# Optimization experiments

Hardware: AMD Instinct MI355X
Metric: run time of the kernel (lower is better)

The kernel has to match this reference:

```python
import jax, jax.numpy as jnp
from jax import lax
import numpy as np

INIT_DIST = 1e10  # matches torch.ones(B,N) * 10000000000.0


def farthest_point_sample(xyz, npoint):
    """xyz: [B, N, 3] float. Returns idx [B, npoint] int32 (RAN=False seed = index 1)."""
    B, N, _ = xyz.shape
    dist0 = jnp.full((B, N), INIT_DIST, dtype=xyz.dtype)
    far0 = jnp.ones((B,), dtype=jnp.int32)  # RAN=False -> torch.randint(1, 2) == 1

    def step(carry, _):
        distance, farthest = carry
        # gather current centroid: [B, 1, 3]
        centroid = jnp.take_along_axis(xyz, farthest[:, None, None].astype(jnp.int32) * jnp.ones((1, 1, 3), jnp.int32), axis=1)
        d = jnp.sum((xyz - centroid) ** 2, axis=-1)        # [B, N]
        distance = jnp.minimum(distance, d)                 # masked update dist < distance
        new_far = jnp.argmax(distance, axis=-1).astype(jnp.int32)
        return (distance, new_far), farthest

    (_, _), idx = lax.scan(step, (dist0, far0), None, length=npoint)
    return idx.T  # [B, npoint]


def index_points(points, idx):
    """points: [B, N, C], idx: [B, S] -> [B, S, C]"""
    B = points.shape[0]
    return points[jnp.arange(B)[:, None], idx]


def setup_inputs() -> dict:
    key = jax.random.key(0)
    xyz = jax.random.normal(key, (32, 32768, 3), dtype=jnp.float32)
    return {"xyz": xyz, "npoint": 4096}


def reference(xyz, npoint):
    idx = farthest_point_sample(xyz, npoint)      # [B, npoint] int32
    sampled = index_points(xyz, idx)              # [B, npoint, 3]
    return idx, sampled
```

## Files before the change

kernel.cpp:

```cpp
#include <hip/hip_runtime.h>


#define BATCH  32
#define NPTS   32768
#define NPOINT 4096
#define NT     1024
#define NCH    16

__global__ __launch_bounds__(NT, 1)
__attribute__((amdgpu_num_vgpr(128)))
void fps_kernel(
    const float* __restrict__ xyz,
    float* __restrict__ out_idx,
    float* __restrict__ out_xyz)
{
#pragma clang fp contract(off)
    __shared__ float pz_lds[NPTS];
    __shared__ unsigned int s_val[3];
    __shared__ int s_idx[3];

    const int b   = blockIdx.x;
    const int tid = threadIdx.x;
    const float* base = xyz + (size_t)b * NPTS * 3;

    float px[NCH * 2], py[NCH * 2], dist[NCH * 2];
#pragma unroll
    for (int c = 0; c < NCH; ++c) {
#pragma unroll
        for (int j = 0; j < 2; ++j) {
            const int i = c * 2 + j;
            const int g = c * 2048 + 2 * tid + j;
            px[i] = base[g * 3 + 0];
            py[i] = base[g * 3 + 1];
            pz_lds[g] = base[g * 3 + 2];
            dist[i] = 1e10f;
        }
    }
    if (tid == 0) {
        s_val[0] = 0u; s_val[1] = 0u; s_val[2] = 0u;
        s_idx[0] = 0x7fffffff; s_idx[1] = 0x7fffffff; s_idx[2] = 0x7fffffff;
    }
    __syncthreads();

    int w = 1;
    int p = 0;

    for (int k = 0; k < NPOINT; ++k) {
        const float cx = base[w * 3 + 0];
        const float cy = base[w * 3 + 1];
        const float cz = base[w * 3 + 2];
        if (tid == 0) {
            out_idx[(size_t)b * NPOINT + k] = (float)w;
            float* o = out_xyz + ((size_t)b * NPOINT + k) * 3;
            o[0] = cx; o[1] = cy; o[2] = cz;
        }

        float best = -1.0f;
        int   lc   = 63;
#pragma unroll
        for (int c = 0; c < NCH; ++c) {
            const float2 zz = *(const float2*)&pz_lds[c * 2048 + 2 * tid];
            const float pzv[2] = { zz.x, zz.y };
#pragma unroll
            for (int j = 0; j < 2; ++j) {
                const int i = c * 2 + j;
                const float dx = px[i] - cx;
                const float dy = py[i] - cy;
                const float dz = pzv[j] - cz;
                const float d  = fmaf(dz, dz, fmaf(dx, dx, dy * dy));
                const float nd = fminf(dist[i], d);
                dist[i] = nd;
                if (nd > best) { best = nd; lc = 2 * c + j; }
            }
        }

        float m = best;
#pragma unroll
        for (int off = 1; off < 64; off <<= 1)
            m = fmaxf(m, __shfl_xor(m, off, 64));
        if ((tid & 63) == 0)
            atomicMax(&s_val[p], __float_as_uint(m));
        __syncthreads();
        const float M = __uint_as_float(s_val[p]);

        if (best == M) {
            const int bi = (lc >> 1) * 2048 + 2 * tid + (lc & 1);
            atomicMin(&s_idx[p], bi);
        }
        __syncthreads();
        w = s_idx[p];
        const int pn2 = (p >= 1) ? (p - 1) : 2;
        if (tid == 0) { s_val[pn2] = 0u; s_idx[pn2] = 0x7fffffff; }
        p = (p == 2) ? 0 : (p + 1);
    }
}

extern "C" void kernel_launch(void* const* d_in, const int* in_sizes, int n_in,
                              void* d_out, int out_size, void* d_ws, size_t ws_size,
                              hipStream_t stream) {
    const float* xyz = (const float*)d_in[0];
    float* out = (float*)d_out;
    float* out_idx = out;
    float* out_xyz = out + (size_t)BATCH * NPOINT;

    fps_kernel<<<BATCH, NT, 0, stream>>>(xyz, out_idx, out_xyz);
}
```

Baseline: 8.764 ms.

## Stream packed xy from workspace each iteration and use DPP wave max

A pre-pass packs x,y into a float2 workspace. The main kernel now reloads x,y from global memory (L2 or cache) with float4 loads on every iteration instead of holding them in registers. This frees VGPRs by dropping the 128-register cap, and the centroid z is read from LDS. The shuffle-based wave max reduction is replaced with DPP row operations, with the reduction result taken from lane 63. A fallback kernel keeps the old register-resident path for when the workspace is too small. The cost is extra global memory traffic inside each of the many serial iterations.

Result: faster. 8.144 ms (-7.1%).

```diff
diff --git a/kernel.cpp b/kernel.cpp
--- a/kernel.cpp
+++ b/kernel.cpp
@@ -6,11 +6,31 @@
 #define NPOINT 4096
 #define NT     1024
 #define NCH    16
-
-__global__ __launch_bounds__(NT, 1)
-__attribute__((amdgpu_num_vgpr(128)))
-void fps_kernel(
+#define WS_NEEDED ((size_t)BATCH * NPTS * 8)
+
+#define DPP1(x, ctrl, rm) __builtin_amdgcn_update_dpp((x), (x), (ctrl), (rm), 0xf, false)
+
+__device__ __forceinline__ float wave_max_dpp(float v) {
+    unsigned int u = __float_as_uint(v);
+    u = __float_as_uint(fmaxf(__uint_as_float(u), __uint_as_float(DPP1(u, 0xB1, 0xf))));
+    u = __float_as_uint(fmaxf(__uint_as_float(u), __uint_as_float(DPP1(u, 0x4E, 0xf))));
+    u = __float_as_uint(fmaxf(__uint_as_float(u), __uint_as_float(DPP1(u, 0x141, 0xf))));
+    u = __float_as_uint(fmaxf(__uint_as_float(u), __uint_as_float(DPP1(u, 0x140, 0xf))));
+    u = __float_as_uint(fmaxf(__uint_as_float(u), __uint_as_float(DPP1(u, 0x142, 0xa))));
+    u = __float_as_uint(fmaxf(__uint_as_float(u), __uint_as_float(DPP1(u, 0x143, 0xc))));
+    return __uint_as_float(u);
+}
+
+__global__ __launch_bounds__(256) void pack_xy(
+    const float* __restrict__ xyz, float2* __restrict__ ws)
+{
+    const int i = blockIdx.x * 256 + threadIdx.x;
+    ws[i] = make_float2(xyz[(size_t)i * 3 + 0], xyz[(size_t)i * 3 + 1]);
+}
+
+__global__ __launch_bounds__(NT, 1) void fps_kernel(
     const float* __restrict__ xyz,
+    const float2* __restrict__ wsxy,
     float* __restrict__ out_idx,
     float* __restrict__ out_xyz)
 {
@@ -22,18 +42,17 @@
     const int b   = blockIdx.x;
     const int tid = threadIdx.x;
     const float* base = xyz + (size_t)b * NPTS * 3;
-
-    float px[NCH * 2], py[NCH * 2], dist[NCH * 2];
+    const float2* xy  = wsxy + (size_t)b * NPTS;
+    const float4* xy4 = (const float4*)xy;
+
+    float dist[NCH * 2];
 #pragma unroll
     for (int c = 0; c < NCH; ++c) {
 #pragma unroll
         for (int j = 0; j < 2; ++j) {
-            const int i = c * 2 + j;
             const int g = c * 2048 + 2 * tid + j;
-            px[i] = base[g * 3 + 0];
-            py[i] = base[g * 3 + 1];
             pz_lds[g] = base[g * 3 + 2];
-            dist[i] = 1e10f;
+            dist[c * 2 + j] = 1e10f;
         }
     }
     if (tid == 0) {
@@ -46,9 +65,9 @@
     int p = 0;
 
     for (int k = 0; k < NPOINT; ++k) {
-        const float cx = base[w * 3 + 0];
-        const float cy = base[w * 3 + 1];
-        const float cz = base[w * 3 + 2];
+        const float2 cxy = xy[w];
+        const float cz = pz_lds[w];
+        const float cx = cxy.x, cy = cxy.y;
         if (tid == 0) {
             out_idx[(size_t)b * NPOINT + k] = (float)w;
             float* o = out_xyz + ((size_t)b * NPOINT + k) * 3;
@@ -59,30 +78,101 @@
         int   lc   = 63;
 #pragma unroll
         for (int c = 0; c < NCH; ++c) {
+            const float4 v  = xy4[c * 1024 + tid];
+            const float2 zz = *(const float2*)&pz_lds[c * 2048 + 2 * tid];
+            {
+                const float dx = v.x - cx;
+                const float dy = v.y - cy;
+                const float dz = zz.x - cz;
+                const float d  = fmaf(dz, dz, fmaf(dx, dx, dy * dy));
+                const float nd = fminf(dist[c * 2 + 0], d);
+                dist[c * 2 + 0] = nd;
+                if (nd > best) { best = nd; lc = 2 * c + 0; }
+            }
+            {
+                const float dx = v.z - cx;
+                const float dy = v.w - cy;
+                const float dz = zz.y - cz;
+                const float d  = fmaf(dz, dz, fmaf(dx, dx, dy * dy));
+                const float nd = fminf(dist[c * 2 + 1], d);
+                dist[c * 2 + 1] = nd;
+                if (nd > best) { best = nd; lc = 2 * c + 1; }
+            }
+        }
+
+        const float m = wave_max_dpp(best);
+        if ((tid & 63) == 63)
+            atomicMax(&s_val[p], __float_as_uint(m));
+        __syncthreads();
+        const float M = __uint_as_float(s_val[p]);
+
+        if (best == M) {
+            const int bi = (lc >> 1) * 2048 + 2 * tid + (lc & 1);
+            atomicMin(&s_idx[p], bi);
+        }
+        __syncthreads();
+        w = s_idx[p];
+        const int pn2 = (p >= 1) ? (p - 1) : 2;
+        if (tid == 0) { s_val[pn2] = 0u; s_idx[pn2] = 0x7fffffff; }
+        p = (p == 2) ? 0 : (p + 1);
+    }
+}
+
+__global__ __launch_bounds__(NT, 1)
+__attribute__((amdgpu_num_vgpr(128)))
+void fps_fallback(
+    const float* __restrict__ xyz, float* __restrict__ out_idx,
+    float* __restrict__ out_xyz)
+{
+#pragma clang fp contract(off)
+    __shared__ float pz_lds[NPTS];
+    __shared__ unsigned int s_val[3];
+    __shared__ int s_idx[3];
+    const int b = blockIdx.x, tid = threadIdx.x;
+    const float* base = xyz + (size_t)b * NPTS * 3;
+    float px[NCH * 2], py[NCH * 2], dist[NCH * 2];
+#pragma unroll
+    for (int c = 0; c < NCH; ++c)
+#pragma unroll
+        for (int j = 0; j < 2; ++j) {
+            const int i = c * 2 + j, g = c * 2048 + 2 * tid + j;
+            px[i] = base[g * 3 + 0]; py[i] = base[g * 3 + 1];
+            pz_lds[g] = base[g * 3 + 2]; dist[i] = 1e10f;
+        }
+    if (tid == 0) {
+        s_val[0] = 0u; s_val[1] = 0u; s_val[2] = 0u;
+        s_idx[0] = 0x7fffffff; s_idx[1] = 0x7fffffff; s_idx[2] = 0x7fffffff;
+    }
+    __syncthreads();
+    int w = 1, p = 0;
+    for (int k = 0; k < NPOINT; ++k) {
+        const float cx = base[w * 3 + 0], cy = base[w * 3 + 1],
+                    cz = base[w * 3 + 2];
+        if (tid == 0) {
+            out_idx[(size_t)b * NPOINT + k] = (float)w;
+            float* o = out_xyz + ((size_t)b * NPOINT + k) * 3;
+            o[0] = cx; o[1] = cy; o[2] = cz;
+        }
+        float best = -1.0f; int lc = 63;
+#pragma unroll
+        for (int c = 0; c < NCH; ++c) {
             const float2 zz = *(const float2*)&pz_lds[c * 2048 + 2 * tid];
             const float pzv[2] = { zz.x, zz.y };
 #pragma unroll
             for (int j = 0; j < 2; ++j) {
                 const int i = c * 2 + j;
-                const float dx = px[i] - cx;
-                const float dy = py[i] - cy;
-                const float dz = pzv[j] - cz;
+                const float dx = px[i] - cx, dy = py[i] - cy,
+                            dz = pzv[j] - cz;
                 const float d  = fmaf(dz, dz, fmaf(dx, dx, dy * dy));
                 const float nd = fminf(dist[i], d);
                 dist[i] = nd;
                 if (nd > best) { best = nd; lc = 2 * c + j; }
             }
         }
-
-        float m = best;
-#pragma unroll
-        for (int off = 1; off < 64; off <<= 1)
-            m = fmaxf(m, __shfl_xor(m, off, 64));
-        if ((tid & 63) == 0)
-            atomicMax(&s_val[p], __float_as_uint(m));
+        const float m = wave_max_dpp(best);
+        if ((tid & 63) == 63) atomicMax(&s_val[p], __float_as_uint(m));
         __syncthreads();
         const float M = __uint_as_float(s_val[p]);
-
         if (best == M) {
             const int bi = (lc >> 1) * 2048 + 2 * tid + (lc & 1);
             atomicMin(&s_idx[p], bi);
@@ -103,5 +193,11 @@
     float* out_idx = out;
     float* out_xyz = out + (size_t)BATCH * NPOINT;
 
-    fps_kernel<<<BATCH, NT, 0, stream>>>(xyz, out_idx, out_xyz);
-}
+    if (ws_size >= WS_NEEDED) {
+        float2* wsxy = (float2*)d_ws;
+        pack_xy<<<(BATCH * NPTS) / 256, 256, 0, stream>>>(xyz, wsxy);
+        fps_kernel<<<BATCH, NT, 0, stream>>>(xyz, wsxy, out_idx, out_xyz);
+    } else {
+        fps_fallback<<<BATCH, NT, 0, stream>>>(xyz, out_idx, out_xyz);
+    }
+}
```

## Stash x/y in AGPRs, use DPP wave max, defer argmax index search

Applied to the files above, without the earlier changes.

Moves the per-thread x and y coordinates into accumulation registers (AGPRs) through inline asm and drops the forced 128-VGPR cap, which relieves VGPR pressure. The inner loop now tracks only a running max and drops the per-element index select; the winning local index is found by rescanning dist only in the threads whose best equals the block max. The wave reduction switches from shuffle_xor to DPP row and broadcast ops, with lane 63 holding the result. The cost is an extra accvgpr read per coordinate in every iteration and a rescan loop in the winning threads.

Result: slower. 9.283 ms (+5.9%).

```diff
diff --git a/kernel.cpp b/kernel.cpp
--- a/kernel.cpp
+++ b/kernel.cpp
@@ -7,9 +7,25 @@
 #define NT     1024
 #define NCH    16
 
-__global__ __launch_bounds__(NT, 1)
-__attribute__((amdgpu_num_vgpr(128)))
-void fps_kernel(
+#define DPP1(x, ctrl, rm) __builtin_amdgcn_update_dpp((x), (x), (ctrl), (rm), 0xf, false)
+
+__device__ __forceinline__ float wave_max_dpp(float v) {
+    unsigned int u = __float_as_uint(v);
+    u = __float_as_uint(fmaxf(__uint_as_float(u), __uint_as_float(DPP1(u, 0xB1, 0xf))));
+    u = __float_as_uint(fmaxf(__uint_as_float(u), __uint_as_float(DPP1(u, 0x4E, 0xf))));
+    u = __float_as_uint(fmaxf(__uint_as_float(u), __uint_as_float(DPP1(u, 0x141, 0xf))));
+    u = __float_as_uint(fmaxf(__uint_as_float(u), __uint_as_float(DPP1(u, 0x140, 0xf))));
+    u = __float_as_uint(fmaxf(__uint_as_float(u), __uint_as_float(DPP1(u, 0x142, 0xa))));
+    u = __float_as_uint(fmaxf(__uint_as_float(u), __uint_as_float(DPP1(u, 0x143, 0xc))));
+    return __uint_as_float(u);
+}
+
+#define AWRITE(dst, src) \
+    asm volatile("v_accvgpr_write_b32 %0, %1" : "=a"(dst) : "v"(src))
+#define AREAD(dst, src) \
+    asm volatile("v_accvgpr_read_b32 %0, %1" : "=v"(dst) : "a"(src))
+
+__global__ __launch_bounds__(NT, 1) void fps_kernel(
     const float* __restrict__ xyz,
     float* __restrict__ out_idx,
     float* __restrict__ out_xyz)
@@ -23,16 +39,19 @@
     const int tid = threadIdx.x;
     const float* base = xyz + (size_t)b * NPTS * 3;
 
-    float px[NCH * 2], py[NCH * 2], dist[NCH * 2];
+    float dist[NCH * 2];
+    float ax[NCH * 2], ay[NCH * 2];
 #pragma unroll
     for (int c = 0; c < NCH; ++c) {
 #pragma unroll
         for (int j = 0; j < 2; ++j) {
             const int i = c * 2 + j;
             const int g = c * 2048 + 2 * tid + j;
-            px[i] = base[g * 3 + 0];
-            py[i] = base[g * 3 + 1];
+            const float x = base[g * 3 + 0];
+            const float y = base[g * 3 + 1];
             pz_lds[g] = base[g * 3 + 2];
+            AWRITE(ax[i], x);
+            AWRITE(ay[i], y);
             dist[i] = 1e10f;
         }
     }
@@ -56,35 +75,46 @@
         }
 
         float best = -1.0f;
-        int   lc   = 63;
 #pragma unroll
         for (int c = 0; c < NCH; ++c) {
+            float x0, y0, x1, y1;
+            AREAD(x0, ax[c * 2 + 0]);
+            AREAD(y0, ay[c * 2 + 0]);
+            AREAD(x1, ax[c * 2 + 1]);
+            AREAD(y1, ay[c * 2 + 1]);
             const float2 zz = *(const float2*)&pz_lds[c * 2048 + 2 * tid];
-            const float pzv[2] = { zz.x, zz.y };
-#pragma unroll
-            for (int j = 0; j < 2; ++j) {
-                const int i = c * 2 + j;
-                const float dx = px[i] - cx;
-                const float dy = py[i] - cy;
-                const float dz = pzv[j] - cz;
+            {
+                const float dx = x0 - cx;
+                const float dy = y0 - cy;
+                const float dz = zz.x - cz;
                 const float d  = fmaf(dz, dz, fmaf(dx, dx, dy * dy));
-                const float nd = fminf(dist[i], d);
-                dist[i] = nd;
-                if (nd > best) { best = nd; lc = 2 * c + j; }
+                const float nd = fminf(dist[c * 2 + 0], d);
+                dist[c * 2 + 0] = nd;
+                best = fmaxf(best, nd);
+            }
+            {
+                const float dx = x1 - cx;
+                const float dy = y1 - cy;
+                const float dz = zz.y - cz;
+                const float d  = fmaf(dz, dz, fmaf(dx, dx, dy * dy));
+                const float nd = fminf(dist[c * 2 + 1], d);
+                dist[c * 2 + 1] = nd;
+                best = fmaxf(best, nd);
             }
         }
 
-        float m = best;
-#pragma unroll
-        for (int off = 1; off < 64; off <<= 1)
-            m = fmaxf(m, __shfl_xor(m, off, 64));
-        if ((tid & 63) == 0)
+        const float m = wave_max_dpp(best);
+        if ((tid & 63) == 63)
             atomicMax(&s_val[p], __float_as_uint(m));
         __syncthreads();
         const float M = __uint_as_float(s_val[p]);
 
         if (best == M) {
-            const int bi = (lc >> 1) * 2048 + 2 * tid + (lc & 1);
+            int li = 63;
+#pragma unroll
+            for (int i = 31; i >= 0; --i)
+                if (dist[i] == M) li = i;
+            const int bi = (li >> 1) * 2048 + 2 * tid + (li & 1);
             atomicMin(&s_idx[p], bi);
         }
         __syncthreads();
```
